# Performance work log

Measured on AMD Instinct MI355X. Metric: run time of the kernel, lower is better.

The kernel has to match this reference:

```python
import jax, jax.numpy as jnp
import numpy as np

N, M, D_MODEL, H, D_K, D_V = 2048, 2048, 1024, 16, 64, 64


def setup_inputs() -> dict:
    key = jax.random.key(0)
    ks = jax.random.split(key, 12)
    s = D_MODEL ** -0.5
    Q = jax.random.normal(ks[0], (N, D_MODEL), dtype=jnp.float32)
    K = jax.random.normal(ks[1], (M, D_MODEL), dtype=jnp.float32)
    V = jax.random.normal(ks[2], (M, D_MODEL), dtype=jnp.float32)
    mask = jnp.ones((N, M), dtype=bool)  # unused by the original forward
    # stacked per-head Linear params (torch Linear: y = x @ W.T + b); here stored as (H, in, out)
    Wq = jax.random.normal(ks[3], (H, D_MODEL, D_K), dtype=jnp.float32) * s
    bq = jax.random.normal(ks[4], (H, D_K), dtype=jnp.float32) * 0.01
    Wk = jax.random.normal(ks[5], (H, D_MODEL, D_K), dtype=jnp.float32) * s
    bk = jax.random.normal(ks[6], (H, D_K), dtype=jnp.float32) * 0.01
    Wv = jax.random.normal(ks[7], (H, D_MODEL, D_V), dtype=jnp.float32) * s
    bv = jax.random.normal(ks[8], (H, D_V), dtype=jnp.float32) * 0.01
    Wo = jax.random.normal(ks[9], (H * D_V, D_MODEL), dtype=jnp.float32) * ((H * D_V) ** -0.5)
    bo = jax.random.normal(ks[10], (D_MODEL,), dtype=jnp.float32) * 0.01
    return dict(Q=Q, K=K, V=V, mask=mask, Wq=Wq, bq=bq, Wk=Wk, bk=bk,
                Wv=Wv, bv=bv, Wo=Wo, bo=bo)


def reference(Q, K, V, mask, Wq, bq, Wk, bk, Wv, bv, Wo, bo):
    # per-head projections, batched over heads (h)
    Qh = jnp.einsum('nd,hdk->hnk', Q, Wq) + bq[:, None, :]  # (H, n, d_k)
    Kh = jnp.einsum('md,hdk->hmk', K, Wk) + bk[:, None, :]  # (H, m, d_k)
    Vh = jnp.einsum('md,hdv->hmv', V, Wv) + bv[:, None, :]  # (H, m, d_v)
    # faithful to source: scale d_k**-0.5 is applied AFTER the softmax
    scores = jnp.einsum('hnk,hmk->hnm', Qh, Kh)             # (H, n, m)
    attn = jax.nn.softmax(scores, axis=-1) * (D_K ** -0.5)
    heads = jnp.einsum('hnm,hmv->hnv', attn, Vh)            # (H, n, d_v)
    concat = jnp.transpose(heads, (1, 0, 2)).reshape(heads.shape[1], H * D_V)
    return concat @ Wo + bo                                  # (n, d_model)
```

## Files before the change

kernel.cpp:

```cpp
#include <hip/hip_runtime.h>

#define N_TOK 2048
#define DMODEL 1024
#define NH 16
#define DK 64
#define SOFF 48.0f

typedef __attribute__((ext_vector_type(8))) short bfrag;
typedef __attribute__((ext_vector_type(4))) float f32x4;
typedef __attribute__((ext_vector_type(16))) float f32x16;
typedef __attribute__((ext_vector_type(4))) unsigned u32x4;

__device__ __forceinline__ unsigned short f2bf(float f) {
    unsigned u = __builtin_bit_cast(unsigned, f);
    u += 0x7FFFu + ((u >> 16) & 1u);
    return (unsigned short)(u >> 16);
}
__device__ __forceinline__ float bf2f(unsigned short u) {
    unsigned x = ((unsigned)u) << 16;
    return __builtin_bit_cast(float, x);
}
__device__ __forceinline__ unsigned cvtpk(float lo, float hi) {
    unsigned r;
    asm volatile("v_cvt_pk_bf16_f32 %0, %1, %2" : "=v"(r) : "v"(lo), "v"(hi));
    return r;
}

__device__ __forceinline__ int swz(int row, int b) {
    return row * 128 + (b ^ ((row & 7) << 4));
}

__device__ __forceinline__ void gload16(const void* g, void* l) {
    __builtin_amdgcn_global_load_lds(
        (__attribute__((address_space(1))) void*)g,
        (__attribute__((address_space(3))) void*)l,
        16, 0, 0);
}

__global__ __launch_bounds__(256) void split_act(
    const float* __restrict__ Qin, const float* __restrict__ Kin, const float* __restrict__ Vin,
    unsigned short* __restrict__ AhQ, unsigned short* __restrict__ AhK, unsigned short* __restrict__ AhV)
{
    const int z = blockIdx.y;
    const float* src = (z == 0) ? Qin : (z == 1) ? Kin : Vin;
    unsigned short* dh = (z == 0) ? AhQ : (z == 1) ? AhK : AhV;

    size_t base = ((size_t)blockIdx.x * 256 + threadIdx.x) * 8;
    float4 a = *reinterpret_cast<const float4*>(src + base);
    float4 b = *reinterpret_cast<const float4*>(src + base + 4);
    float f[8] = {a.x, a.y, a.z, a.w, b.x, b.y, b.z, b.w};
    unsigned short hb[8];
    #pragma unroll
    for (int i = 0; i < 8; ++i) hb[i] = f2bf(f[i]);
    *reinterpret_cast<uint4*>(dh + base) = *reinterpret_cast<const uint4*>(hb);
}

__global__ __launch_bounds__(256) void split_w(
    const float* __restrict__ Wq_, const float* __restrict__ Wk_, const float* __restrict__ Wv_,
    unsigned short* __restrict__ Wth0, unsigned short* __restrict__ Wth1, unsigned short* __restrict__ Wth2,
    unsigned short* __restrict__ Wtl0, unsigned short* __restrict__ Wtl1)
{
    const int z = blockIdx.z;
    const float* W = (z == 0) ? Wq_ : (z == 1) ? Wk_ : Wv_;
    unsigned short* oh = (z == 0) ? Wth0 : (z == 1) ? Wth1 : Wth2;
    unsigned short* ol = (z == 0) ? Wtl0 : (z == 1) ? Wtl1 : nullptr;
    const int h = blockIdx.y, dt = blockIdx.x;
    const int tid = threadIdx.x;

    __shared__ float lds[64][65];

    {
        int rr = tid >> 2, c4 = (tid & 3) * 16;
        const float* src = W + ((size_t)h * DMODEL + dt * 64 + rr) * DK + c4;
        #pragma unroll
        for (int i = 0; i < 4; ++i) {
            float4 v = *reinterpret_cast<const float4*>(src + i * 4);
            lds[rr][c4 + i * 4 + 0] = v.x;
            lds[rr][c4 + i * 4 + 1] = v.y;
            lds[rr][c4 + i * 4 + 2] = v.z;
            lds[rr][c4 + i * 4 + 3] = v.w;
        }
    }
    __syncthreads();
    {
        int kk_ = tid >> 2, d4 = (tid & 3) * 16;
        unsigned short hb[16], lb[16];
        #pragma unroll
        for (int i = 0; i < 16; ++i) {
            float v = lds[d4 + i][kk_];
            hb[i] = f2bf(v);
            lb[i] = f2bf(v - bf2f(hb[i]));
        }
        size_t o = (size_t)(h * 64 + kk_) * DMODEL + dt * 64 + d4;
        *reinterpret_cast<uint4*>(oh + o)     = *reinterpret_cast<const uint4*>(hb);
        *reinterpret_cast<uint4*>(oh + o + 8) = *reinterpret_cast<const uint4*>(hb + 8);
        if (z < 2) {
            *reinterpret_cast<uint4*>(ol + o)     = *reinterpret_cast<const uint4*>(lb);
            *reinterpret_cast<uint4*>(ol + o + 8) = *reinterpret_cast<const uint4*>(lb + 8);
        }
    }
}

__global__ __launch_bounds__(256) void split_wo(
    const float* __restrict__ Wo, unsigned short* __restrict__ WoT)
{
    const int dt = blockIdx.x, jt = blockIdx.y;
    const int tid = threadIdx.x;
    __shared__ float lds[64][65];

    {
        int rr = tid >> 2, c4 = (tid & 3) * 16;
        const float* src = Wo + (size_t)(dt * 64 + rr) * DMODEL + jt * 64 + c4;
        #pragma unroll
        for (int i = 0; i < 4; ++i) {
            float4 v = *reinterpret_cast<const float4*>(src + i * 4);
            lds[rr][c4 + i * 4 + 0] = v.x;
            lds[rr][c4 + i * 4 + 1] = v.y;
            lds[rr][c4 + i * 4 + 2] = v.z;
            lds[rr][c4 + i * 4 + 3] = v.w;
        }
    }
    __syncthreads();
    {
        int jj = tid >> 2, d4 = (tid & 3) * 16;
        unsigned short hb[16];
        #pragma unroll
        for (int i = 0; i < 16; ++i) hb[i] = f2bf(lds[d4 + i][jj]);
        size_t o = (size_t)(jt * 64 + jj) * DMODEL + dt * 64 + d4;
        *reinterpret_cast<uint4*>(WoT + o)     = *reinterpret_cast<const uint4*>(hb);
        *reinterpret_cast<uint4*>(WoT + o + 8) = *reinterpret_cast<const uint4*>(hb + 8);
    }
}

__global__ __launch_bounds__(256) void proj_kernel(
    const unsigned short* __restrict__ AhQ, const unsigned short* __restrict__ AhK, const unsigned short* __restrict__ AhV,
    const unsigned short* __restrict__ WthQ, const unsigned short* __restrict__ WthK, const unsigned short* __restrict__ WthV,
    const unsigned short* __restrict__ WtlQ, const unsigned short* __restrict__ WtlK,
    const float* __restrict__ bq_, const float* __restrict__ bk_, const float* __restrict__ bv_,
    unsigned short* __restrict__ Qhh,
    unsigned short* __restrict__ Khh,
    unsigned short* __restrict__ Vt)
{
    const int z = blockIdx.z;
    const unsigned short* Ah = (z == 0) ? AhK : (z == 1) ? AhQ : AhV;
    const unsigned short* Bh = (z == 0) ? WthK : (z == 1) ? WthQ : WthV;
    const unsigned short* Bl = (z == 0) ? WtlK : WtlQ;
    const float* bias = (z == 0) ? bk_ : (z == 1) ? bq_ : bv_;

    __shared__ alignas(16) unsigned char sAh[16384];
    __shared__ alignas(16) unsigned char sBh[16384];
    __shared__ alignas(16) unsigned char sBl[16384];

    const int tid = threadIdx.x;
    const int lane = tid & 63;
    const int w = tid >> 6;
    const int wm = w >> 1, wn = w & 1;
    const int g = lane >> 4, li = lane & 15;

    const int row0 = blockIdx.x * 128;
    const int col0 = blockIdx.y * 128;

    f32x4 acc[4][4];
    #pragma unroll
    for (int m = 0; m < 4; ++m)
        #pragma unroll
        for (int n = 0; n < 4; ++n) acc[m][n] = f32x4{0.f, 0.f, 0.f, 0.f};

    for (int kt = 0; kt < DMODEL; kt += 64) {
        __syncthreads();
        #pragma unroll
        for (int p = 0; p < 4; ++p) {
            int chunk = p * 256 + tid;
            int r = chunk >> 3, cc = chunk & 7;
            int cs = (cc * 8) ^ ((r & 7) << 3);
            int ldso = (p * 256 + w * 64) * 16;
            gload16(Ah + (size_t)(row0 + r) * DMODEL + kt + cs, sAh + ldso);
            gload16(Bh + (size_t)(col0 + r) * DMODEL + kt + cs, sBh + ldso);
            if (z < 2)
                gload16(Bl + (size_t)(col0 + r) * DMODEL + kt + cs, sBl + ldso);
        }
        __syncthreads();

        if (z < 2) {
            #pragma unroll
            for (int kk = 0; kk < 2; ++kk) {
                bfrag afh[4], bfh[4], bfl[4];
                #pragma unroll
                for (int m = 0; m < 4; ++m)
                    afh[m] = *reinterpret_cast<const bfrag*>(sAh + swz(wm * 64 + m * 16 + li, kk * 64 + g * 16));
                #pragma unroll
                for (int n = 0; n < 4; ++n) {
                    bfh[n] = *reinterpret_cast<const bfrag*>(sBh + swz(wn * 64 + n * 16 + li, kk * 64 + g * 16));
                    bfl[n] = *reinterpret_cast<const bfrag*>(sBl + swz(wn * 64 + n * 16 + li, kk * 64 + g * 16));
                }
                #pragma unroll
                for (int m = 0; m < 4; ++m)
                    #pragma unroll
                    for (int n = 0; n < 4; ++n) {
                        acc[m][n] = __builtin_amdgcn_mfma_f32_16x16x32_bf16(afh[m], bfh[n], acc[m][n], 0, 0, 0);
                        acc[m][n] = __builtin_amdgcn_mfma_f32_16x16x32_bf16(afh[m], bfl[n], acc[m][n], 0, 0, 0);
                    }
            }
        } else {
            #pragma unroll
            for (int kk = 0; kk < 2; ++kk) {
                bfrag afh[4], bfh[4];
                #pragma unroll
                for (int m = 0; m < 4; ++m)
                    afh[m] = *reinterpret_cast<const bfrag*>(sAh + swz(wm * 64 + m * 16 + li, kk * 64 + g * 16));
                #pragma unroll
                for (int n = 0; n < 4; ++n)
                    bfh[n] = *reinterpret_cast<const bfrag*>(sBh + swz(wn * 64 + n * 16 + li, kk * 64 + g * 16));
                #pragma unroll
                for (int m = 0; m < 4; ++m)
                    #pragma unroll
                    for (int n = 0; n < 4; ++n)
                        acc[m][n] = __builtin_amdgcn_mfma_f32_16x16x32_bf16(afh[m], bfh[n], acc[m][n], 0, 0, 0);
            }
        }
    }

    #pragma unroll
    for (int m = 0; m < 4; ++m) {
        #pragma unroll
        for (int n = 0; n < 4; ++n) {
            int colg = col0 + wn * 64 + n * 16 + li;
            float bb = bias[colg];
            int hh = colg >> 6, k = colg & 63;
            int rowb = row0 + wm * 64 + m * 16 + g * 4;
            if (z == 2) {
                unsigned short vb4[4];
                #pragma unroll
                for (int r = 0; r < 4; ++r) vb4[r] = f2bf(acc[m][n][r] + bb);
                *reinterpret_cast<uint2*>(Vt + ((size_t)hh * DK + k) * N_TOK + rowb) =
                    *reinterpret_cast<const uint2*>(vb4);
            } else {
                #pragma unroll
                for (int r = 0; r < 4; ++r) {
                    size_t o = ((size_t)hh * N_TOK + rowb + r) * DK + k;
                    float val = acc[m][n][r] + bb;
                    if (z == 1) val *= 1.44269504088896f;
                    if (z == 0) Khh[o] = f2bf(val);
                    else        Qhh[o] = f2bf(val);
                }
            }
        }
    }
}

__global__ __launch_bounds__(256) void attn_kernel(
    const unsigned short* __restrict__ Qhh,
    const unsigned short* __restrict__ Khh,
    const unsigned short* __restrict__ Vt,
    unsigned short* __restrict__ Opart, float* __restrict__ lbuf)
{
    __shared__ alignas(16) unsigned char sKh[3][8192];
    __shared__ alignas(16) unsigned char sV [3][8192];

    const int bid = blockIdx.x;
    const int orig = (bid & 7) * 64 + (bid >> 3);
    const int h    = orig >> 5;
    const int half = (orig >> 4) & 1;
    const int qt   = orig & 15;

    const int tid  = threadIdx.x;
    const int lane = tid & 63;
    const int w    = tid >> 6;
    const int q31  = lane & 31;
    const int hi   = lane >> 5;
    const int qrow0 = qt * 128 + w * 32;

    const unsigned short* QbH = Qhh + (size_t)h * N_TOK * DK;
    const unsigned short* KbH = Khh + (size_t)h * N_TOK * DK;
    const unsigned short* Vtb = Vt  + (size_t)h * DK * N_TOK;

    bfrag bqh[4];
    #pragma unroll
    for (int d = 0; d < 4; ++d)
        bqh[d] = *reinterpret_cast<const bfrag*>(
            QbH + (size_t)(qrow0 + q31) * DK + d * 16 + hi * 8);

    f32x16 acc0 = {}, acc1 = {};
    float lrun = 0.f;

    const int tbase = half * (N_TOK / 2);

#define STAGE(B, T) do {                                                     \
    _Pragma("unroll")                                                        \
    for (int p_ = 0; p_ < 2; ++p_) {                                         \
        int chunk_ = p_ * 256 + w * 64 + lane;                               \
        int r_ = chunk_ >> 3;                                                \
        int cs_ = ((chunk_ & 7) * 8) ^ ((r_ & 7) << 3);                      \
        int ldso_ = (p_ * 256 + w * 64) * 16;                                \
        gload16(KbH + (size_t)((T) + r_) * DK + cs_, sKh[B] + ldso_);        \
        gload16(Vtb + (size_t)r_ * N_TOK + (T) + cs_, sV[B] + ldso_);        \
    } } while (0)

#define MKFRAG(W, PF) do {                                                   \
    _Pragma("unroll")                                                        \
    for (int kk_ = 0; kk_ < 2; ++kk_) {                                      \
        unsigned b0_ = W[4 * kk_ + 0], b1_ = W[4 * kk_ + 1];                 \
        unsigned a0_ = W[4 * kk_ + 2], a1_ = W[4 * kk_ + 3];                 \
        unsigned sb0_ = (unsigned)__shfl_xor((int)b0_, 32);                  \
        unsigned sa0_ = (unsigned)__shfl_xor((int)a0_, 32);                  \
        unsigned sb1_ = (unsigned)__shfl_xor((int)b1_, 32);                  \
        unsigned sa1_ = (unsigned)__shfl_xor((int)a1_, 32);                  \
        u32x4 t_ = { hi ? sa0_ : b0_, hi ? sa1_ : b1_,                       \
                     hi ? a0_ : sb0_, hi ? a1_ : sb1_ };                     \
        PF[kk_] = __builtin_bit_cast(bfrag, t_);                             \
    } } while (0)

    STAGE(0, tbase);

    int cur = 0;
    for (int tt = 0; tt < 16; ++tt) {
        int nxt = cur + 1; if (nxt == 3) nxt = 0;
        if (tt < 15) {
            STAGE(nxt, tbase + (tt + 1) * 64);
            asm volatile("s_waitcnt vmcnt(4)" ::: "memory");
        } else {
            asm volatile("s_waitcnt vmcnt(0)" ::: "memory");
        }
        __builtin_amdgcn_s_barrier();
        asm volatile("" ::: "memory");

        f32x16 s0, s1;
        #pragma unroll
        for (int r = 0; r < 16; ++r) { s0[r] = -SOFF; s1[r] = -SOFF; }
        __builtin_amdgcn_s_setprio(1);
        #pragma unroll
        for (int d = 0; d < 4; ++d) {
            const int bo = d * 32 + hi * 16;
            bfrag kh0 = *reinterpret_cast<const bfrag*>(sKh[cur] + swz(q31,      bo));
            bfrag kh1 = *reinterpret_cast<const bfrag*>(sKh[cur] + swz(32 + q31, bo));
            s0 = __builtin_amdgcn_mfma_f32_32x32x16_bf16(kh0, bqh[d], s0, 0, 0, 0);
            s1 = __builtin_amdgcn_mfma_f32_32x32x16_bf16(kh1, bqh[d], s1, 0, 0, 0);
        }
        __builtin_amdgcn_s_setprio(0);

        float p0[16], p1[16];
        #pragma unroll
        for (int r = 0; r < 16; ++r) p0[r] = __builtin_exp2f(s0[r]);
        #pragma unroll
        for (int r = 0; r < 16; ++r) p1[r] = __builtin_exp2f(s1[r]);
        float ps = ((p0[0] + p0[1]) + (p0[2] + p0[3])) + ((p0[4] + p0[5]) + (p0[6] + p0[7]))
                 + ((p0[8] + p0[9]) + (p0[10] + p0[11])) + ((p0[12] + p0[13]) + (p0[14] + p0[15]))
                 + ((p1[0] + p1[1]) + (p1[2] + p1[3])) + ((p1[4] + p1[5]) + (p1[6] + p1[7]))
                 + ((p1[8] + p1[9]) + (p1[10] + p1[11])) + ((p1[12] + p1[13]) + (p1[14] + p1[15]));
        ps += __shfl_xor(ps, 32);
        lrun += ps;

        unsigned w0[8], w1[8];
        #pragma unroll
        for (int j = 0; j < 8; ++j) w0[j] = cvtpk(p0[2 * j], p0[2 * j + 1]);
        #pragma unroll
        for (int j = 0; j < 8; ++j) w1[j] = cvtpk(p1[2 * j], p1[2 * j + 1]);
        bfrag pf0[2], pf1[2];
        MKFRAG(w0, pf0);
        MKFRAG(w1, pf1);

        __builtin_amdgcn_s_setprio(1);
        #pragma unroll
        for (int ks = 0; ks < 4; ++ks) {
            bfrag pb = (ks < 2) ? pf0[ks & 1] : pf1[ks & 1];
            const int bo = ks * 32 + hi * 16;
            bfrag va0 = *reinterpret_cast<const bfrag*>(sV[cur] + swz(q31,      bo));
            bfrag va1 = *reinterpret_cast<const bfrag*>(sV[cur] + swz(32 + q31, bo));
            acc0 = __builtin_amdgcn_mfma_f32_32x32x16_bf16(va0, pb, acc0, 0, 0, 0);
            acc1 = __builtin_amdgcn_mfma_f32_32x32x16_bf16(va1, pb, acc1, 0, 0, 0);
        }
        __builtin_amdgcn_s_setprio(0);
        asm volatile("" ::: "memory");
        cur = nxt;
    }
#undef STAGE
#undef MKFRAG

    const size_t idxp = (size_t)half * NH * N_TOK + (size_t)h * N_TOK + qrow0 + q31;
    unsigned short* op = Opart + idxp * 64;
    #pragma unroll
    for (int m = 0; m < 4; ++m) {
        uint2 wa = make_uint2(cvtpk(acc0[4 * m], acc0[4 * m + 1]),
                              cvtpk(acc0[4 * m + 2], acc0[4 * m + 3]));
        uint2 wb = make_uint2(cvtpk(acc1[4 * m], acc1[4 * m + 1]),
                              cvtpk(acc1[4 * m + 2], acc1[4 * m + 3]));
        *reinterpret_cast<uint2*>(op + 8 * m + 4 * hi)      = wa;
        *reinterpret_cast<uint2*>(op + 32 + 8 * m + 4 * hi) = wb;
    }
    if (lane < 32)
        lbuf[idxp] = lrun;
}

__global__ __launch_bounds__(256) void combine_kernel(
    const unsigned short* __restrict__ Opart, const float* __restrict__ lbuf,
    unsigned short* __restrict__ Hc)
{
    const int tid = threadIdx.x;
    const int sub = tid & 3;
    const int idx = blockIdx.x * 64 + (tid >> 2);
    const int h = idx >> 11, row = idx & 2047;
    const int HS = NH * N_TOK;

    float inv = 0.125f / (lbuf[idx] + lbuf[HS + idx]);

    const unsigned short* O1 = Opart + (size_t)idx * 64 + sub * 16;
    const unsigned short* O2 = Opart + ((size_t)HS + idx) * 64 + sub * 16;
    uint4 x1 = *reinterpret_cast<const uint4*>(O1);
    uint4 y1 = *reinterpret_cast<const uint4*>(O1 + 8);
    uint4 x2 = *reinterpret_cast<const uint4*>(O2);
    uint4 y2 = *reinterpret_cast<const uint4*>(O2 + 8);
    unsigned wa[8] = {x1.x, x1.y, x1.z, x1.w, y1.x, y1.y, y1.z, y1.w};
    unsigned wb[8] = {x2.x, x2.y, x2.z, x2.w, y2.x, y2.y, y2.z, y2.w};
    unsigned short hb[16];
    #pragma unroll
    for (int j = 0; j < 8; ++j) {
        float lo = (bf2f((unsigned short)(wa[j] & 0xFFFF)) +
                    bf2f((unsigned short)(wb[j] & 0xFFFF))) * inv;
        float hi2 = (bf2f((unsigned short)(wa[j] >> 16)) +
                     bf2f((unsigned short)(wb[j] >> 16))) * inv;
        hb[2 * j]     = f2bf(lo);
        hb[2 * j + 1] = f2bf(hi2);
    }
    size_t o = (size_t)row * DMODEL + h * 64 + sub * 16;
    *reinterpret_cast<uint4*>(Hc + o)     = *reinterpret_cast<const uint4*>(hb);
    *reinterpret_cast<uint4*>(Hc + o + 8) = *reinterpret_cast<const uint4*>(hb + 8);
}

__global__ __launch_bounds__(256) void oproj_kernel(
    const unsigned short* __restrict__ Hc,
    const unsigned short* __restrict__ WoT,
    const float* __restrict__ bo,
    float* __restrict__ out)
{
    __shared__ alignas(16) unsigned char sA[8192];
    __shared__ alignas(16) unsigned char sB[16384];

    const int tid = threadIdx.x;
    const int lane = tid & 63;
    const int w = tid >> 6;
    const int wm = w >> 1, wn = w & 1;
    const int g = lane >> 4, li = lane & 15;
    const int row0 = blockIdx.x * 64;
    const int col0 = blockIdx.y * 128;

    f32x4 acc[2][4];
    #pragma unroll
    for (int m = 0; m < 2; ++m)
        #pragma unroll
        for (int n = 0; n < 4; ++n) acc[m][n] = f32x4{0.f, 0.f, 0.f, 0.f};

    for (int kt = 0; kt < DMODEL; kt += 64) {
        __syncthreads();
        #pragma unroll
        for (int p = 0; p < 2; ++p) {
            int chunk = p * 256 + tid;
            int r = chunk >> 3, cc = chunk & 7;
            int cs = (cc * 8) ^ ((r & 7) << 3);
            int ldso = (p * 256 + w * 64) * 16;
            gload16(Hc + (size_t)(row0 + r) * DMODEL + kt + cs, sA + ldso);
        }
        #pragma unroll
        for (int p = 0; p < 4; ++p) {
            int chunk = p * 256 + tid;
            int r = chunk >> 3, cc = chunk & 7;
            int cs = (cc * 8) ^ ((r & 7) << 3);
            int ldso = (p * 256 + w * 64) * 16;
            gload16(WoT + (size_t)(col0 + r) * DMODEL + kt + cs, sB + ldso);
        }
        __syncthreads();

        #pragma unroll
        for (int kk = 0; kk < 2; ++kk) {
            bfrag af[2], bf_[4];
            #pragma unroll
            for (int m = 0; m < 2; ++m)
                af[m] = *reinterpret_cast<const bfrag*>(sA + swz(wm * 32 + m * 16 + li, kk * 64 + g * 16));
            #pragma unroll
            for (int n = 0; n < 4; ++n)
                bf_[n] = *reinterpret_cast<const bfrag*>(sB + swz(wn * 64 + n * 16 + li, kk * 64 + g * 16));
            #pragma unroll
            for (int m = 0; m < 2; ++m)
                #pragma unroll
                for (int n = 0; n < 4; ++n)
                    acc[m][n] = __builtin_amdgcn_mfma_f32_16x16x32_bf16(af[m], bf_[n], acc[m][n], 0, 0, 0);
        }
    }

    #pragma unroll
    for (int m = 0; m < 2; ++m) {
        #pragma unroll
        for (int n = 0; n < 4; ++n) {
            int colg = col0 + wn * 64 + n * 16 + li;
            float bb = bo[colg];
            #pragma unroll
            for (int r = 0; r < 4; ++r) {
                int rowg = row0 + wm * 32 + m * 16 + g * 4 + r;
                out[(size_t)rowg * DMODEL + colg] = acc[m][n][r] + bb;
            }
        }
    }
}

extern "C" void kernel_launch(void* const* d_in, const int* in_sizes, int n_in,
                              void* d_out, int out_size, void* d_ws, size_t ws_size,
                              hipStream_t stream) {
    (void)in_sizes; (void)n_in; (void)out_size; (void)ws_size;
    const float* Q  = (const float*)d_in[0];
    const float* K  = (const float*)d_in[1];
    const float* V  = (const float*)d_in[2];
    const float* Wq = (const float*)d_in[4];
    const float* bq = (const float*)d_in[5];
    const float* Wk = (const float*)d_in[6];
    const float* bk = (const float*)d_in[7];
    const float* Wv = (const float*)d_in[8];
    const float* bv = (const float*)d_in[9];
    const float* Wo = (const float*)d_in[10];
    const float* bo = (const float*)d_in[11];
    float* out = (float*)d_out;

    const size_t ASZ = (size_t)N_TOK * DMODEL;
    const size_t WSZ = (size_t)NH * DK * DMODEL;
    const size_t HSZ = (size_t)NH * N_TOK * DK;
    unsigned short* p = (unsigned short*)d_ws;
    unsigned short* AhQ = p; p += ASZ;
    unsigned short* AhK = p; p += ASZ;
    unsigned short* AhV = p; p += ASZ;
    unsigned short* WthQ = p; p += WSZ;
    unsigned short* WthK = p; p += WSZ;
    unsigned short* WthV = p; p += WSZ;
    unsigned short* WtlQ = p; p += WSZ;
    unsigned short* WtlK = p; p += WSZ;
    unsigned short* Qhh = p; p += HSZ;
    unsigned short* Khh = p; p += HSZ;
    unsigned short* Vt  = p; p += HSZ;
    unsigned short* Hc  = p; p += HSZ;
    unsigned short* WoT = p; p += ASZ / 2;

    unsigned short* Opart = (unsigned short*)d_ws;
    float* lbuf = (float*)(Opart + (size_t)2 * NH * N_TOK * 64);

    split_act<<<dim3(1024, 3), 256, 0, stream>>>(Q, K, V, AhQ, AhK, AhV);
    split_w<<<dim3(16, 16, 3), 256, 0, stream>>>(Wq, Wk, Wv, WthQ, WthK, WthV, WtlQ, WtlK);
    split_wo<<<dim3(16, 16), 256, 0, stream>>>(Wo, WoT);
    proj_kernel<<<dim3(16, 8, 3), 256, 0, stream>>>(
        AhQ, AhK, AhV, WthQ, WthK, WthV, WtlQ, WtlK,
        bq, bk, bv, Qhh, Khh, Vt);
    attn_kernel<<<dim3(512), 256, 0, stream>>>(Qhh, Khh, Vt, Opart, lbuf);
    combine_kernel<<<dim3(512), 256, 0, stream>>>(Opart, lbuf, Hc);
    oproj_kernel<<<dim3(32, 8), 256, 0, stream>>>(Hc, WoT, bo, out);
}
```

Before: 108.3 us.

## Split attention keys into four partitions and merge prep kernels into one launch

The attention kernel now splits each head's key range into four quarters instead of two, launching 1024 blocks instead of 512. Each block runs half as many KV tile iterations, and the combine kernel sums four partial outputs and row sums. The three weight and activation conversion kernels are fused into one prep kernel dispatched by block index, which removes two kernel launches. In exchange, partial-output traffic to the combine stage doubles and the Opart workspace grows; it still fits below the Q/K/V head buffers it aliases.

```diff
diff --git a/kernel.cpp b/kernel.cpp
--- a/kernel.cpp
+++ b/kernel.cpp
@@ -37,98 +37,94 @@
         16, 0, 0);
 }
 
-__global__ __launch_bounds__(256) void split_act(
+__global__ __launch_bounds__(256) void prep_kernel(
     const float* __restrict__ Qin, const float* __restrict__ Kin, const float* __restrict__ Vin,
-    unsigned short* __restrict__ AhQ, unsigned short* __restrict__ AhK, unsigned short* __restrict__ AhV)
+    const float* __restrict__ Wq_, const float* __restrict__ Wk_, const float* __restrict__ Wv_,
+    const float* __restrict__ Wo_,
+    unsigned short* __restrict__ AhQ, unsigned short* __restrict__ AhK, unsigned short* __restrict__ AhV,
+    unsigned short* __restrict__ WthQ, unsigned short* __restrict__ WthK, unsigned short* __restrict__ WthV,
+    unsigned short* __restrict__ WtlQ, unsigned short* __restrict__ WtlK,
+    unsigned short* __restrict__ WoT)
 {
-    const int z = blockIdx.y;
-    const float* src = (z == 0) ? Qin : (z == 1) ? Kin : Vin;
-    unsigned short* dh = (z == 0) ? AhQ : (z == 1) ? AhK : AhV;
-
-    size_t base = ((size_t)blockIdx.x * 256 + threadIdx.x) * 8;
-    float4 a = *reinterpret_cast<const float4*>(src + base);
-    float4 b = *reinterpret_cast<const float4*>(src + base + 4);
-    float f[8] = {a.x, a.y, a.z, a.w, b.x, b.y, b.z, b.w};
-    unsigned short hb[8];
-    #pragma unroll
-    for (int i = 0; i < 8; ++i) hb[i] = f2bf(f[i]);
-    *reinterpret_cast<uint4*>(dh + base) = *reinterpret_cast<const uint4*>(hb);
-}
-
-__global__ __launch_bounds__(256) void split_w(
-    const float* __restrict__ Wq_, const float* __restrict__ Wk_, const float* __restrict__ Wv_,
-    unsigned short* __restrict__ Wth0, unsigned short* __restrict__ Wth1, unsigned short* __restrict__ Wth2,
-    unsigned short* __restrict__ Wtl0, unsigned short* __restrict__ Wtl1)
-{
-    const int z = blockIdx.z;
-    const float* W = (z == 0) ? Wq_ : (z == 1) ? Wk_ : Wv_;
-    unsigned short* oh = (z == 0) ? Wth0 : (z == 1) ? Wth1 : Wth2;
-    unsigned short* ol = (z == 0) ? Wtl0 : (z == 1) ? Wtl1 : nullptr;
-    const int h = blockIdx.y, dt = blockIdx.x;
-    const int tid = threadIdx.x;
-
-    __shared__ float lds[64][65];
-
-    {
-        int rr = tid >> 2, c4 = (tid & 3) * 16;
-        const float* src = W + ((size_t)h * DMODEL + dt * 64 + rr) * DK + c4;
-        #pragma unroll
-        for (int i = 0; i < 4; ++i) {
-            float4 v = *reinterpret_cast<const float4*>(src + i * 4);
-            lds[rr][c4 + i * 4 + 0] = v.x;
-            lds[rr][c4 + i * 4 + 1] = v.y;
-            lds[rr][c4 + i * 4 + 2] = v.z;
-            lds[rr][c4 + i * 4 + 3] = v.w;
-        }
-    }
-    __syncthreads();
-    {
-        int kk_ = tid >> 2, d4 = (tid & 3) * 16;
-        unsigned short hb[16], lb[16];
-        #pragma unroll
-        for (int i = 0; i < 16; ++i) {
-            float v = lds[d4 + i][kk_];
-            hb[i] = f2bf(v);
-            lb[i] = f2bf(v - bf2f(hb[i]));
-        }
-        size_t o = (size_t)(h * 64 + kk_) * DMODEL + dt * 64 + d4;
-        *reinterpret_cast<uint4*>(oh + o)     = *reinterpret_cast<const uint4*>(hb);
-        *reinterpret_cast<uint4*>(oh + o + 8) = *reinterpret_cast<const uint4*>(hb + 8);
-        if (z < 2) {
-            *reinterpret_cast<uint4*>(ol + o)     = *reinterpret_cast<const uint4*>(lb);
-            *reinterpret_cast<uint4*>(ol + o + 8) = *reinterpret_cast<const uint4*>(lb + 8);
-        }
-    }
-}
-
-__global__ __launch_bounds__(256) void split_wo(
-    const float* __restrict__ Wo, unsigned short* __restrict__ WoT)
-{
-    const int dt = blockIdx.x, jt = blockIdx.y;
+    const int bid = blockIdx.x;
     const int tid = threadIdx.x;
     __shared__ float lds[64][65];
 
-    {
-        int rr = tid >> 2, c4 = (tid & 3) * 16;
-        const float* src = Wo + (size_t)(dt * 64 + rr) * DMODEL + jt * 64 + c4;
-        #pragma unroll
-        for (int i = 0; i < 4; ++i) {
-            float4 v = *reinterpret_cast<const float4*>(src + i * 4);
-            lds[rr][c4 + i * 4 + 0] = v.x;
-            lds[rr][c4 + i * 4 + 1] = v.y;
-            lds[rr][c4 + i * 4 + 2] = v.z;
-            lds[rr][c4 + i * 4 + 3] = v.w;
-        }
-    }
-    __syncthreads();
-    {
-        int jj = tid >> 2, d4 = (tid & 3) * 16;
-        unsigned short hb[16];
-        #pragma unroll
-        for (int i = 0; i < 16; ++i) hb[i] = f2bf(lds[d4 + i][jj]);
-        size_t o = (size_t)(jt * 64 + jj) * DMODEL + dt * 64 + d4;
-        *reinterpret_cast<uint4*>(WoT + o)     = *reinterpret_cast<const uint4*>(hb);
-        *reinterpret_cast<uint4*>(WoT + o + 8) = *reinterpret_cast<const uint4*>(hb + 8);
+    if (bid < 3072) {
+        const int z = bid >> 10, x = bid & 1023;
+        const float* src = (z == 0) ? Qin : (z == 1) ? Kin : Vin;
+        unsigned short* dh = (z == 0) ? AhQ : (z == 1) ? AhK : AhV;
+        size_t base = ((size_t)x * 256 + tid) * 8;
+        float4 a = *reinterpret_cast<const float4*>(src + base);
+        float4 b = *reinterpret_cast<const float4*>(src + base + 4);
+        float f[8] = {a.x, a.y, a.z, a.w, b.x, b.y, b.z, b.w};
+        unsigned short hb[8];
+        #pragma unroll
+        for (int i = 0; i < 8; ++i) hb[i] = f2bf(f[i]);
+        *reinterpret_cast<uint4*>(dh + base) = *reinterpret_cast<const uint4*>(hb);
+    } else if (bid < 3840) {
+        const int t = bid - 3072;
+        const int z = t >> 8, rem = t & 255;
+        const int h = rem >> 4, dt = rem & 15;
+        const float* W = (z == 0) ? Wq_ : (z == 1) ? Wk_ : Wv_;
+        unsigned short* oh = (z == 0) ? WthQ : (z == 1) ? WthK : WthV;
+        unsigned short* ol = (z == 0) ? WtlQ : WtlK;
+
+        {
+            int rr = tid >> 2, c4 = (tid & 3) * 16;
+            const float* src = W + ((size_t)h * DMODEL + dt * 64 + rr) * DK + c4;
+            #pragma unroll
+            for (int i = 0; i < 4; ++i) {
+                float4 v = *reinterpret_cast<const float4*>(src + i * 4);
+                lds[rr][c4 + i * 4 + 0] = v.x;
+                lds[rr][c4 + i * 4 + 1] = v.y;
+                lds[rr][c4 + i * 4 + 2] = v.z;
+                lds[rr][c4 + i * 4 + 3] = v.w;
+            }
+        }
+        __syncthreads();
+        {
+            int kk_ = tid >> 2, d4 = (tid & 3) * 16;
+            unsigned short hb[16], lb[16];
+            #pragma unroll
+            for (int i = 0; i < 16; ++i) {
+                float v = lds[d4 + i][kk_];
+                hb[i] = f2bf(v);
+                lb[i] = f2bf(v - bf2f(hb[i]));
+            }
+            size_t o = (size_t)(h * 64 + kk_) * DMODEL + dt * 64 + d4;
+            *reinterpret_cast<uint4*>(oh + o)     = *reinterpret_cast<const uint4*>(hb);
+            *reinterpret_cast<uint4*>(oh + o + 8) = *reinterpret_cast<const uint4*>(hb + 8);
+            if (z < 2) {
+                *reinterpret_cast<uint4*>(ol + o)     = *reinterpret_cast<const uint4*>(lb);
+                *reinterpret_cast<uint4*>(ol + o + 8) = *reinterpret_cast<const uint4*>(lb + 8);
+            }
+        }
+    } else {
+        const int t = bid - 3840;
+        const int dt = t >> 4, jt = t & 15;
+        {
+            int rr = tid >> 2, c4 = (tid & 3) * 16;
+            const float* src = Wo_ + (size_t)(dt * 64 + rr) * DMODEL + jt * 64 + c4;
+            #pragma unroll
+            for (int i = 0; i < 4; ++i) {
+                float4 v = *reinterpret_cast<const float4*>(src + i * 4);
+                lds[rr][c4 + i * 4 + 0] = v.x;
+                lds[rr][c4 + i * 4 + 1] = v.y;
+                lds[rr][c4 + i * 4 + 2] = v.z;
+                lds[rr][c4 + i * 4 + 3] = v.w;
+            }
+        }
+        __syncthreads();
+        {
+            int jj = tid >> 2, d4 = (tid & 3) * 16;
+            unsigned short hb[16];
+            #pragma unroll
+            for (int i = 0; i < 16; ++i) hb[i] = f2bf(lds[d4 + i][jj]);
+            size_t o = (size_t)(jt * 64 + jj) * DMODEL + dt * 64 + d4;
+            *reinterpret_cast<uint4*>(WoT + o)     = *reinterpret_cast<const uint4*>(hb);
+            *reinterpret_cast<uint4*>(WoT + o + 8) = *reinterpret_cast<const uint4*>(hb + 8);
+        }
     }
 }
 
@@ -258,10 +254,10 @@
     __shared__ alignas(16) unsigned char sV [3][8192];
 
     const int bid = blockIdx.x;
-    const int orig = (bid & 7) * 64 + (bid >> 3);
-    const int h    = orig >> 5;
-    const int half = (orig >> 4) & 1;
-    const int qt   = orig & 15;
+    const int orig = (bid & 7) * 128 + (bid >> 3);
+    const int h       = orig >> 6;
+    const int quarter = (orig >> 4) & 3;
+    const int qt      = orig & 15;
 
     const int tid  = threadIdx.x;
     const int lane = tid & 63;
@@ -283,7 +279,7 @@
     f32x16 acc0 = {}, acc1 = {};
     float lrun = 0.f;
 
-    const int tbase = half * (N_TOK / 2);
+    const int tbase = quarter * (N_TOK / 4);
 
 #define STAGE(B, T) do {                                                     \
     _Pragma("unroll")                                                        \
@@ -313,9 +309,9 @@
     STAGE(0, tbase);
 
     int cur = 0;
-    for (int tt = 0; tt < 16; ++tt) {
+    for (int tt = 0; tt < 8; ++tt) {
         int nxt = cur + 1; if (nxt == 3) nxt = 0;
-        if (tt < 15) {
+        if (tt < 7) {
             STAGE(nxt, tbase + (tt + 1) * 64);
             asm volatile("s_waitcnt vmcnt(4)" ::: "memory");
         } else {
@@ -376,7 +372,7 @@
 #undef STAGE
 #undef MKFRAG
 
-    const size_t idxp = (size_t)half * NH * N_TOK + (size_t)h * N_TOK + qrow0 + q31;
+    const size_t idxp = (size_t)quarter * NH * N_TOK + (size_t)h * N_TOK + qrow0 + q31;
     unsigned short* op = Opart + idxp * 64;
     #pragma unroll
     for (int m = 0; m < 4; ++m) {
@@ -399,28 +395,31 @@
     const int sub = tid & 3;
     const int idx = blockIdx.x * 64 + (tid >> 2);
     const int h = idx >> 11, row = idx & 2047;
-    const int HS = NH * N_TOK;
-
-    float inv = 0.125f / (lbuf[idx] + lbuf[HS + idx]);
-
-    const unsigned short* O1 = Opart + (size_t)idx * 64 + sub * 16;
-    const unsigned short* O2 = Opart + ((size_t)HS + idx) * 64 + sub * 16;
-    uint4 x1 = *reinterpret_cast<const uint4*>(O1);
-    uint4 y1 = *reinterpret_cast<const uint4*>(O1 + 8);
-    uint4 x2 = *reinterpret_cast<const uint4*>(O2);
-    uint4 y2 = *reinterpret_cast<const uint4*>(O2 + 8);
-    unsigned wa[8] = {x1.x, x1.y, x1.z, x1.w, y1.x, y1.y, y1.z, y1.w};
-    unsigned wb[8] = {x2.x, x2.y, x2.z, x2.w, y2.x, y2.y, y2.z, y2.w};
+    const int QS = NH * N_TOK;
+
+    float lsum = 0.f;
+    #pragma unroll
+    for (int q = 0; q < 4; ++q) lsum += lbuf[(size_t)q * QS + idx];
+    float inv = 0.125f / lsum;
+
+    float acc[16];
+    #pragma unroll
+    for (int i = 0; i < 16; ++i) acc[i] = 0.f;
+    #pragma unroll
+    for (int q = 0; q < 4; ++q) {
+        const unsigned short* Oq = Opart + ((size_t)q * QS + idx) * 64 + sub * 16;
+        uint4 x = *reinterpret_cast<const uint4*>(Oq);
+        uint4 y = *reinterpret_cast<const uint4*>(Oq + 8);
+        unsigned wds[8] = {x.x, x.y, x.z, x.w, y.x, y.y, y.z, y.w};
+        #pragma unroll
+        for (int j = 0; j < 8; ++j) {
+            acc[2 * j]     += bf2f((unsigned short)(wds[j] & 0xFFFF));
+            acc[2 * j + 1] += bf2f((unsigned short)(wds[j] >> 16));
+        }
+    }
     unsigned short hb[16];
     #pragma unroll
-    for (int j = 0; j < 8; ++j) {
-        float lo = (bf2f((unsigned short)(wa[j] & 0xFFFF)) +
-                    bf2f((unsigned short)(wb[j] & 0xFFFF))) * inv;
-        float hi2 = (bf2f((unsigned short)(wa[j] >> 16)) +
-                     bf2f((unsigned short)(wb[j] >> 16))) * inv;
-        hb[2 * j]     = f2bf(lo);
-        hb[2 * j + 1] = f2bf(hi2);
-    }
+    for (int i = 0; i < 16; ++i) hb[i] = f2bf(acc[i] * inv);
     size_t o = (size_t)row * DMODEL + h * 64 + sub * 16;
     *reinterpret_cast<uint4*>(Hc + o)     = *reinterpret_cast<const uint4*>(hb);
     *reinterpret_cast<uint4*>(Hc + o + 8) = *reinterpret_cast<const uint4*>(hb + 8);
@@ -537,15 +536,15 @@
     unsigned short* WoT = p; p += ASZ / 2;
 
     unsigned short* Opart = (unsigned short*)d_ws;
-    float* lbuf = (float*)(Opart + (size_t)2 * NH * N_TOK * 64);
-
-    split_act<<<dim3(1024, 3), 256, 0, stream>>>(Q, K, V, AhQ, AhK, AhV);
-    split_w<<<dim3(16, 16, 3), 256, 0, stream>>>(Wq, Wk, Wv, WthQ, WthK, WthV, WtlQ, WtlK);
-    split_wo<<<dim3(16, 16), 256, 0, stream>>>(Wo, WoT);
+    float* lbuf = (float*)(Opart + (size_t)4 * NH * N_TOK * 64);
+
+    prep_kernel<<<dim3(4096), 256, 0, stream>>>(
+        Q, K, V, Wq, Wk, Wv, Wo,
+        AhQ, AhK, AhV, WthQ, WthK, WthV, WtlQ, WtlK, WoT);
     proj_kernel<<<dim3(16, 8, 3), 256, 0, stream>>>(
         AhQ, AhK, AhV, WthQ, WthK, WthV, WtlQ, WtlK,
         bq, bk, bv, Qhh, Khh, Vt);
-    attn_kernel<<<dim3(512), 256, 0, stream>>>(Qhh, Khh, Vt, Opart, lbuf);
+    attn_kernel<<<dim3(1024), 256, 0, stream>>>(Qhh, Khh, Vt, Opart, lbuf);
     combine_kernel<<<dim3(512), 256, 0, stream>>>(Opart, lbuf, Hc);
     oproj_kernel<<<dim3(32, 8), 256, 0, stream>>>(Hc, WoT, bo, out);
 }
```

Result: faster. 105.8 us (-2.3%).
